# Performance work log

Measured on AMD Instinct MI355X. Metric: run time of the kernel, lower is better.

The kernel has to match this reference:

```python
import jax, jax.numpy as jnp
import numpy as np

N_NODES = 50000
N_EDGES = 800000
D_IN = 256
D_HID = 256
N_CLASSES = 10
N_GRAPHS = 512
LN_EPS = 1e-5


def gcn_conv(x, edge_index, W, b, num_nodes):
    # PyG GCNConv (default settings): h = x @ W; add self-loops; symmetric
    # deg^{-1/2} normalization; sum-aggregate messages; add bias.
    h = x @ W                                   # [N, H]
    loop = jnp.arange(num_nodes, dtype=edge_index.dtype)
    src = jnp.concatenate([edge_index[0], loop])  # [E+N]
    dst = jnp.concatenate([edge_index[1], loop])  # [E+N]
    deg = jax.ops.segment_sum(jnp.ones_like(dst, dtype=h.dtype), dst,
                              num_segments=num_nodes)
    dinv = jnp.where(deg > 0, jax.lax.rsqrt(deg), 0.0)
    norm = dinv[src] * dinv[dst]                # [E+N]
    msg = h[src] * norm[:, None]                # gather + scale
    out = jax.ops.segment_sum(msg, dst, num_segments=num_nodes)  # scatter-add
    return out + b


def layer_norm(x, w, b):
    mu = jnp.mean(x, axis=-1, keepdims=True)
    var = jnp.mean(jnp.square(x - mu), axis=-1, keepdims=True)
    return (x - mu) * jax.lax.rsqrt(var + LN_EPS) * w + b


def global_mean_pool(x, batch, num_graphs):
    s = jax.ops.segment_sum(x, batch, num_segments=num_graphs)
    cnt = jax.ops.segment_sum(jnp.ones_like(batch, dtype=x.dtype), batch,
                              num_segments=num_graphs)
    return s / jnp.maximum(cnt, 1.0)[:, None]


def setup_inputs() -> dict:
    key = jax.random.key(0)
    ks = jax.random.split(key, 12)
    x = jax.random.normal(ks[0], (N_NODES, D_IN), dtype=jnp.float32)
    edge_index = jax.random.randint(ks[1], (2, N_EDGES), 0, N_NODES, dtype=jnp.int32)
    batch = jnp.sort(jax.random.randint(ks[2], (N_NODES,), 0, N_GRAPHS, dtype=jnp.int32))
    s_in = 1.0 / np.sqrt(D_IN)
    s_hid = 1.0 / np.sqrt(D_HID)
    return {
        "x": x,
        "edge_index": edge_index,
        "batch": batch,
        "W1": jax.random.uniform(ks[3], (D_IN, D_HID), jnp.float32, -s_in, s_in),
        "b1": jnp.zeros((D_HID,), jnp.float32),
        "W2": jax.random.uniform(ks[4], (D_HID, D_HID), jnp.float32, -s_hid, s_hid),
        "b2": jnp.zeros((D_HID,), jnp.float32),
        "ln1_w": jnp.ones((D_HID,), jnp.float32),
        "ln1_b": jnp.zeros((D_HID,), jnp.float32),
        "ln2_w": jnp.ones((D_HID,), jnp.float32),
        "ln2_b": jnp.zeros((D_HID,), jnp.float32),
        "lin_W": jax.random.uniform(ks[5], (D_HID, N_CLASSES), jnp.float32, -s_hid, s_hid),
        "lin_b": jnp.zeros((N_CLASSES,), jnp.float32),
    }


def reference(x, edge_index, batch, W1, b1, W2, b2, ln1_w, ln1_b, ln2_w, ln2_b, lin_W, lin_b):
    # dropout is identity at inference (training=False)
    h = gcn_conv(x, edge_index, W1, b1, N_NODES)
    h = jax.nn.relu(layer_norm(h, ln1_w, ln1_b))
    h = gcn_conv(h, edge_index, W2, b2, N_NODES)
    h = jax.nn.relu(layer_norm(h, ln2_w, ln2_b))
    pooled = global_mean_pool(h, batch, N_GRAPHS)   # [G, H]
    return pooled @ lin_W + lin_b                   # [G, C]
```

## Files before the change

### kernel.cpp

```cpp
#include <hip/hip_runtime.h>
#include <hip/hip_fp8.h>
#include <stdint.h>

#define D 256
#define CAP 64

typedef __attribute__((ext_vector_type(8))) short short8;
typedef __attribute__((ext_vector_type(4))) float f32x4;

#define SW2(n, c) (((n) << 7) + ((((c) ^ ((n) & 7))) << 3))

__device__ inline unsigned short f2bf(float f) {
    uint32_t u = __builtin_bit_cast(uint32_t, f);
    uint32_t r = (u + 0x7FFFu + ((u >> 16) & 1u)) >> 16;
    return (unsigned short)r;
}

__device__ inline float bf2f(unsigned short b) {
    return __builtin_bit_cast(float, (uint32_t)b << 16);
}

__device__ inline f32x4 fp8x4_to_f32(uint32_t v) {
    __hip_fp8x4_e4m3 a;
    a.__x = v;
    float4 f = (float4)a;
    return (f32x4){f.x, f.y, f.z, f.w};
}

__device__ inline uint8_t f32_to_fp8(float f) {
    __hip_fp8_e4m3 q(f);
    return (uint8_t)q.__x;
}

__global__ __launch_bounds__(256) void k_prep(const float* __restrict__ x,
                                              unsigned short* __restrict__ xb, int n8,
                                              const float* __restrict__ W1,
                                              const float* __restrict__ W2,
                                              unsigned short* __restrict__ Wt1,
                                              unsigned short* __restrict__ Wt2,
                                              int* __restrict__ cur,
                                              int nNodes, int nf2b) {
    int b = blockIdx.x, t = threadIdx.x;
    if (b < nf2b) {
        int i = b * 256 + t;
        if (i < n8) {
            f32x4 v0 = ((const f32x4*)x)[i * 2];
            f32x4 v1 = ((const f32x4*)x)[i * 2 + 1];
            short8 o;
            o[0] = (short)f2bf(v0.x); o[1] = (short)f2bf(v0.y);
            o[2] = (short)f2bf(v0.z); o[3] = (short)f2bf(v0.w);
            o[4] = (short)f2bf(v1.x); o[5] = (short)f2bf(v1.y);
            o[6] = (short)f2bf(v1.z); o[7] = (short)f2bf(v1.w);
            ((short8*)xb)[i] = o;
        }
    } else if (b < nf2b + 512) {
        int idx = (b - nf2b) * 256 + t;
        int w = idx >> 16;
        int r = idx & 65535;
        int n = r >> 8, k = r & 255;
        const float* W = w ? W2 : W1;
        unsigned short* Wt = w ? Wt2 : Wt1;
        Wt[n * 256 + k] = f2bf(W[k * 256 + n]);
    } else {
        int i = (b - nf2b - 512) * 256 + t;
        if (i < nNodes) cur[i] = 0;
    }
}


__device__ __forceinline__ void gemm_body(unsigned short* sm, int gid,
                                          const unsigned short* __restrict__ A,
                                          const unsigned short* __restrict__ Bt,
                                          uint8_t* __restrict__ Cb, int M) {
    int t = threadIdx.x;
    int wave = t >> 6, lane = t & 63;
    int quad = lane >> 4, l16 = lane & 15;
    int mr = wave >> 1, nc = wave & 1;
    int bm = (gid >> 1) * 128;
    int bn = (gid & 1) * 128;

    uint4 af[4][8];
#pragma unroll
    for (int tm = 0; tm < 4; ++tm) {
        int row = bm + mr * 64 + tm * 16 + l16;
        if (row >= M) row = M - 1;
        const unsigned short* ap = A + (size_t)row * D + quad * 8;
#pragma unroll
        for (int ks = 0; ks < 8; ++ks)
            af[tm][ks] = *reinterpret_cast<const uint4*>(ap + ks * 32);
    }

    f32x4 acc[4][4];
#pragma unroll
    for (int tm = 0; tm < 4; ++tm)
#pragma unroll
        for (int tn = 0; tn < 4; ++tn) acc[tm][tn] = (f32x4){0.f, 0.f, 0.f, 0.f};

#pragma unroll
    for (int half = 0; half < 2; ++half) {
        {
            int c = t & 15;
            int r0 = t >> 4;
#pragma unroll
            for (int j = 0; j < 8; ++j) {
                int r = r0 + j * 16;
                uint4 v = *reinterpret_cast<const uint4*>(
                    Bt + (size_t)(bn + r) * D + half * 128 + c * 8);
                *reinterpret_cast<uint4*>(sm + SW2(r, c)) = v;
            }
        }
        __syncthreads();
#pragma unroll
        for (int ks = 0; ks < 4; ++ks) {
            int gks = half * 4 + ks;
            short8 b[4];
#pragma unroll
            for (int tn = 0; tn < 4; ++tn) {
                int n = nc * 64 + tn * 16 + l16;
                b[tn] = *reinterpret_cast<const short8*>(sm + SW2(n, ks * 4 + quad));
            }
#pragma unroll
            for (int tm = 0; tm < 4; ++tm) {
                short8 a = __builtin_bit_cast(short8, af[tm][gks]);
#pragma unroll
                for (int tn = 0; tn < 4; ++tn)
                    acc[tm][tn] = __builtin_amdgcn_mfma_f32_16x16x32_bf16(a, b[tn], acc[tm][tn], 0, 0, 0);
            }
        }
        __syncthreads();
    }

    uint8_t (*sC)[136] = reinterpret_cast<uint8_t (*)[136]>(sm);
#pragma unroll
    for (int tm = 0; tm < 4; ++tm) {
        int rb = mr * 64 + tm * 16 + quad * 4;
#pragma unroll
        for (int tn = 0; tn < 4; ++tn) {
            int cc = nc * 64 + tn * 16 + l16;
#pragma unroll
            for (int r = 0; r < 4; ++r)
                sC[rb + r][cc] = f32_to_fp8(acc[tm][tn][r]);
        }
    }
    __syncthreads();

#pragma unroll
    for (int it = 0; it < 4; ++it) {
        int idx = it * 256 + t;
        int r = idx >> 3, ch = idx & 7;
        int gr = bm + r;
        if (gr < M)
            *reinterpret_cast<uint4*>(Cb + (size_t)gr * D + bn + ch * 16) =
                *reinterpret_cast<const uint4*>(&sC[r][ch * 16]);
    }
}

__device__ __forceinline__ void fill_body(int fid,
                                          const int* __restrict__ src,
                                          const int* __restrict__ dst,
                                          int* __restrict__ cur,
                                          int* __restrict__ ewi, int ne) {
    int i = (fid * 256 + threadIdx.x) * 4;
    if (i + 4 <= ne) {
        int4 s4 = *reinterpret_cast<const int4*>(src + i);
        int4 d4 = *reinterpret_cast<const int4*>(dst + i);
        int p;
        p = atomicAdd(&cur[d4.x], 1);
        if (p < CAP) ewi[d4.x * CAP + p] = s4.x;
        p = atomicAdd(&cur[d4.y], 1);
        if (p < CAP) ewi[d4.y * CAP + p] = s4.y;
        p = atomicAdd(&cur[d4.z], 1);
        if (p < CAP) ewi[d4.z * CAP + p] = s4.z;
        p = atomicAdd(&cur[d4.w], 1);
        if (p < CAP) ewi[d4.w * CAP + p] = s4.w;
    } else {
        for (int j = i; j < ne; ++j) {
            int s = src[j], d = dst[j];
            int p = atomicAdd(&cur[d], 1);
            if (p < CAP) ewi[d * CAP + p] = s;
        }
    }
}

__global__ __launch_bounds__(256, 2) void k_gemmfill(const unsigned short* __restrict__ A,
                                                     const unsigned short* __restrict__ Bt,
                                                     uint8_t* __restrict__ Cb, int M,
                                                     const int* __restrict__ src,
                                                     const int* __restrict__ dst,
                                                     int* __restrict__ cur,
                                                     int* __restrict__ ewi, int ne,
                                                     int NI, int ngemm) {
    __shared__ unsigned short sm[16384];
    int b = blockIdx.x;
    if (b < 2 * NI) {
        if (b & 1) fill_body(b >> 1, src, dst, cur, ewi, ne);
        else       gemm_body(sm, b >> 1, A, Bt, Cb, M);
    } else {
        int r = b - 2 * NI;
        if (ngemm > NI) gemm_body(sm, NI + r, A, Bt, Cb, M);
        else            fill_body(NI + r, src, dst, cur, ewi, ne);
    }
}

__global__ __launch_bounds__(256, 2) void k_gemm(const unsigned short* __restrict__ A,
                                                 const unsigned short* __restrict__ Bt,
                                                 uint8_t* __restrict__ Cb, int M) {
    __shared__ unsigned short sm[16384];
    gemm_body(sm, blockIdx.x, A, Bt, Cb, M);
}

__global__ __launch_bounds__(256) void k_agg(const uint8_t* __restrict__ hb,
                                             const int* __restrict__ cur,
                                             const int* __restrict__ ewi,
                                             const float* __restrict__ bias,
                                             const float* __restrict__ lnw,
                                             const float* __restrict__ lnb,
                                             unsigned short* __restrict__ out, int n) {
    __shared__ int2 lew[4][CAP];
    int wave = threadIdx.x >> 6, lane = threadIdx.x & 63;
    int node = blockIdx.x * 4 + wave;
    if (node >= n) return;
    int cdeg = cur[node];
    int cnt = min(cdeg, CAP);
    if (lane < cnt) {
        int s = ewi[node * CAP + lane];
        int2 p;
        p.x = s * 64;
        p.y = __builtin_bit_cast(int, rsqrtf((float)(cur[s] + 1)));
        lew[wave][lane] = p;
    }
    __builtin_amdgcn_wave_barrier();

    float di = rsqrtf((float)(cdeg + 1));
    const uint32_t* hb32 = (const uint32_t*)hb;
    uint32_t rs = hb32[(uint32_t)node * 64 + lane];
    f32x4 acc = (f32x4){0.f, 0.f, 0.f, 0.f};
    const int2* lep = lew[wave];
    int nq = cnt >> 2;

    int2 p0, p1, p2, p3;
    if (nq > 0) { p0 = lep[0]; p1 = lep[1]; p2 = lep[2]; p3 = lep[3]; }
    int q = 0;
#pragma unroll 1
    for (; q + 1 < nq; ++q) {
        int b4 = (q + 1) * 4;
        uint32_t r0 = hb32[(uint32_t)(p0.x + lane)];
        uint32_t r1 = hb32[(uint32_t)(p1.x + lane)];
        uint32_t r2 = hb32[(uint32_t)(p2.x + lane)];
        uint32_t r3 = hb32[(uint32_t)(p3.x + lane)];
        int2 n0 = lep[b4], n1 = lep[b4 + 1], n2 = lep[b4 + 2], n3 = lep[b4 + 3];
        acc += fp8x4_to_f32(r0) * __builtin_bit_cast(float, p0.y);
        acc += fp8x4_to_f32(r1) * __builtin_bit_cast(float, p1.y);
        acc += fp8x4_to_f32(r2) * __builtin_bit_cast(float, p2.y);
        acc += fp8x4_to_f32(r3) * __builtin_bit_cast(float, p3.y);
        p0 = n0; p1 = n1; p2 = n2; p3 = n3;
    }
    if (nq > 0) {
        uint32_t r0 = hb32[(uint32_t)(p0.x + lane)];
        uint32_t r1 = hb32[(uint32_t)(p1.x + lane)];
        uint32_t r2 = hb32[(uint32_t)(p2.x + lane)];
        uint32_t r3 = hb32[(uint32_t)(p3.x + lane)];
        acc += fp8x4_to_f32(r0) * __builtin_bit_cast(float, p0.y);
        acc += fp8x4_to_f32(r1) * __builtin_bit_cast(float, p1.y);
        acc += fp8x4_to_f32(r2) * __builtin_bit_cast(float, p2.y);
        acc += fp8x4_to_f32(r3) * __builtin_bit_cast(float, p3.y);
    }
    for (int e = nq * 4; e < cnt; ++e) {
        int2 p = lep[e];
        uint32_t r = hb32[(uint32_t)(p.x + lane)];
        acc += fp8x4_to_f32(r) * __builtin_bit_cast(float, p.y);
    }

    f32x4 self = fp8x4_to_f32(rs);
    f32x4 b4v = ((const f32x4*)bias)[lane];
    f32x4 v = self * (di * di) + acc * di + b4v;

    float s1 = v.x + v.y + v.z + v.w;
    float s2 = v.x * v.x + v.y * v.y + v.z * v.z + v.w * v.w;
#pragma unroll
    for (int o = 32; o > 0; o >>= 1) {
        s1 += __shfl_xor(s1, o, 64);
        s2 += __shfl_xor(s2, o, 64);
    }
    float mean = s1 * (1.0f / 256.0f);
    float var = s2 * (1.0f / 256.0f) - mean * mean;
    float inv = rsqrtf(var + 1e-5f);
    f32x4 w4 = ((const f32x4*)lnw)[lane];
    f32x4 lb = ((const f32x4*)lnb)[lane];
    float y0 = fmaxf((v.x - mean) * inv * w4.x + lb.x, 0.f);
    float y1 = fmaxf((v.y - mean) * inv * w4.y + lb.y, 0.f);
    float y2 = fmaxf((v.z - mean) * inv * w4.z + lb.z, 0.f);
    float y3 = fmaxf((v.w - mean) * inv * w4.w + lb.w, 0.f);
    uint2 w;
    w.x = (uint32_t)f2bf(y0) | ((uint32_t)f2bf(y1) << 16);
    w.y = (uint32_t)f2bf(y2) | ((uint32_t)f2bf(y3) << 16);
    *reinterpret_cast<uint2*>(out + (size_t)node * D + lane * 4) = w;
}

__global__ __launch_bounds__(256) void k_pool(const unsigned short* __restrict__ h,
                                              const int* __restrict__ batch,
                                              const float* __restrict__ linW,
                                              const float* __restrict__ linb,
                                              float* __restrict__ out,
                                              int nNodes) {
    int g = blockIdx.x, t = threadIdx.x;
    int lo = 0, hi = nNodes;
    while (lo < hi) { int m = (lo + hi) >> 1; if (batch[m] < g) lo = m + 1; else hi = m; }
    int lo2 = lo, hi2 = nNodes;
    while (lo2 < hi2) { int m = (lo2 + hi2) >> 1; if (batch[m] < g + 1) lo2 = m + 1; else hi2 = m; }
    float s0 = 0.f, s1 = 0.f, s2 = 0.f, s3 = 0.f;
    int i = lo;
    for (; i + 4 <= lo2; i += 4) {
        s0 += bf2f(h[(size_t)(i + 0) * D + t]);
        s1 += bf2f(h[(size_t)(i + 1) * D + t]);
        s2 += bf2f(h[(size_t)(i + 2) * D + t]);
        s3 += bf2f(h[(size_t)(i + 3) * D + t]);
    }
    for (; i < lo2; ++i) s0 += bf2f(h[(size_t)i * D + t]);
    float s = (s0 + s1) + (s2 + s3);
    float cnt = (float)(lo2 - lo);
    float pooled = s / fmaxf(cnt, 1.f);
    __shared__ float sp[256];
    __shared__ float red[4];
    sp[t] = pooled;
    __syncthreads();
    for (int c = 0; c < 10; ++c) {
        float v = sp[t] * linW[t * 10 + c];
#pragma unroll
        for (int o = 32; o > 0; o >>= 1) v += __shfl_xor(v, o, 64);
        if ((t & 63) == 0) red[t >> 6] = v;
        __syncthreads();
        if (t == 0) out[g * 10 + c] = red[0] + red[1] + red[2] + red[3] + linb[c];
        __syncthreads();
    }
}

extern "C" void kernel_launch(void* const* d_in, const int* in_sizes, int n_in,
                              void* d_out, int out_size, void* d_ws, size_t ws_size,
                              hipStream_t stream) {
    const float* x    = (const float*)d_in[0];
    const int*   ei   = (const int*)d_in[1];
    const int*   batch= (const int*)d_in[2];
    const float* W1   = (const float*)d_in[3];
    const float* b1   = (const float*)d_in[4];
    const float* W2   = (const float*)d_in[5];
    const float* b2   = (const float*)d_in[6];
    const float* ln1w = (const float*)d_in[7];
    const float* ln1b = (const float*)d_in[8];
    const float* ln2w = (const float*)d_in[9];
    const float* ln2b = (const float*)d_in[10];
    const float* linW = (const float*)d_in[11];
    const float* linb = (const float*)d_in[12];
    float* out = (float*)d_out;

    int nNodes  = in_sizes[0] / D;
    int nEdges  = in_sizes[1] / 2;
    int nGraphs = out_size / 10;

    const int* src = ei;
    const int* dst = ei + nEdges;

    char* ws = (char*)d_ws;
    size_t o = 0;
    auto alloc = [&](size_t bytes) -> char* {
        char* p = ws + o;
        o += (bytes + 511) & ~(size_t)511;
        return p;
    };
    unsigned short* xb = (unsigned short*)alloc((size_t)nNodes * D * 2);
    uint8_t* hW = (uint8_t*)alloc((size_t)nNodes * D);
    unsigned short* h1 = (unsigned short*)alloc((size_t)nNodes * D * 2);
    int* cur   = (int*)alloc((size_t)nNodes * 4);
    int* ewi   = (int*)alloc((size_t)nNodes * CAP * 4);
    unsigned short* Wt1 = (unsigned short*)alloc((size_t)D * D * 2);
    unsigned short* Wt2 = (unsigned short*)alloc((size_t)D * D * 2);
    (void)ws_size;

    int gn = (nNodes + 255) / 256;
    int ge4 = (nEdges / 4 + 255) / 256;
    int n8 = nNodes * (D / 8);
    int nf2b = (n8 + 255) / 256;
    int ngemm = ((nNodes + 127) / 128) * 2;
    int NI = min(ngemm, ge4);

    k_prep<<<nf2b + 512 + gn, 256, 0, stream>>>(x, xb, n8, W1, W2, Wt1, Wt2,
                                                cur, nNodes, nf2b);
    k_gemmfill<<<ngemm + ge4, 256, 0, stream>>>(xb, Wt1, hW, nNodes,
                                                src, dst, cur, ewi, nEdges,
                                                NI, ngemm);
    k_agg<<<(nNodes + 3) / 4, 256, 0, stream>>>(hW, cur, ewi,
                                                b1, ln1w, ln1b, h1, nNodes);
    k_gemm<<<ngemm, 256, 0, stream>>>(h1, Wt2, hW, nNodes);
    k_agg<<<(nNodes + 3) / 4, 256, 0, stream>>>(hW, cur, ewi,
                                                b2, ln2w, ln2b, xb, nNodes);
    k_pool<<<nGraphs, 256, 0, stream>>>(xb, batch, linW, linb, out, nNodes);
}
```

Before: 269.6 us.

## Overlap edge fill with input conversion instead of with the first GEMM

Clearing the degree counters moves from the prep kernel to a hipMemsetAsync. The edge-bucketing fill now runs in one kernel alongside the x-to-bf16 conversion and weight transposes, instead of being interleaved with the first GEMM. The first GEMM becomes a plain k_gemm launch. The aim is to co-schedule the atomic-heavy fill with bandwidth-bound conversion work and let the GEMM run alone at its own occupancy, at the cost of one extra launch plus a memset.

```diff
diff --git a/kernel.cpp b/kernel.cpp
--- a/kernel.cpp
+++ b/kernel.cpp
@@ -30,129 +30,6 @@
 __device__ inline uint8_t f32_to_fp8(float f) {
     __hip_fp8_e4m3 q(f);
     return (uint8_t)q.__x;
-}
-
-__global__ __launch_bounds__(256) void k_prep(const float* __restrict__ x,
-                                              unsigned short* __restrict__ xb, int n8,
-                                              const float* __restrict__ W1,
-                                              const float* __restrict__ W2,
-                                              unsigned short* __restrict__ Wt1,
-                                              unsigned short* __restrict__ Wt2,
-                                              int* __restrict__ cur,
-                                              int nNodes, int nf2b) {
-    int b = blockIdx.x, t = threadIdx.x;
-    if (b < nf2b) {
-        int i = b * 256 + t;
-        if (i < n8) {
-            f32x4 v0 = ((const f32x4*)x)[i * 2];
-            f32x4 v1 = ((const f32x4*)x)[i * 2 + 1];
-            short8 o;
-            o[0] = (short)f2bf(v0.x); o[1] = (short)f2bf(v0.y);
-            o[2] = (short)f2bf(v0.z); o[3] = (short)f2bf(v0.w);
-            o[4] = (short)f2bf(v1.x); o[5] = (short)f2bf(v1.y);
-            o[6] = (short)f2bf(v1.z); o[7] = (short)f2bf(v1.w);
-            ((short8*)xb)[i] = o;
-        }
-    } else if (b < nf2b + 512) {
-        int idx = (b - nf2b) * 256 + t;
-        int w = idx >> 16;
-        int r = idx & 65535;
-        int n = r >> 8, k = r & 255;
-        const float* W = w ? W2 : W1;
-        unsigned short* Wt = w ? Wt2 : Wt1;
-        Wt[n * 256 + k] = f2bf(W[k * 256 + n]);
-    } else {
-        int i = (b - nf2b - 512) * 256 + t;
-        if (i < nNodes) cur[i] = 0;
-    }
-}
-
-
-__device__ __forceinline__ void gemm_body(unsigned short* sm, int gid,
-                                          const unsigned short* __restrict__ A,
-                                          const unsigned short* __restrict__ Bt,
-                                          uint8_t* __restrict__ Cb, int M) {
-    int t = threadIdx.x;
-    int wave = t >> 6, lane = t & 63;
-    int quad = lane >> 4, l16 = lane & 15;
-    int mr = wave >> 1, nc = wave & 1;
-    int bm = (gid >> 1) * 128;
-    int bn = (gid & 1) * 128;
-
-    uint4 af[4][8];
-#pragma unroll
-    for (int tm = 0; tm < 4; ++tm) {
-        int row = bm + mr * 64 + tm * 16 + l16;
-        if (row >= M) row = M - 1;
-        const unsigned short* ap = A + (size_t)row * D + quad * 8;
-#pragma unroll
-        for (int ks = 0; ks < 8; ++ks)
-            af[tm][ks] = *reinterpret_cast<const uint4*>(ap + ks * 32);
-    }
-
-    f32x4 acc[4][4];
-#pragma unroll
-    for (int tm = 0; tm < 4; ++tm)
-#pragma unroll
-        for (int tn = 0; tn < 4; ++tn) acc[tm][tn] = (f32x4){0.f, 0.f, 0.f, 0.f};
-
-#pragma unroll
-    for (int half = 0; half < 2; ++half) {
-        {
-            int c = t & 15;
-            int r0 = t >> 4;
-#pragma unroll
-            for (int j = 0; j < 8; ++j) {
-                int r = r0 + j * 16;
-                uint4 v = *reinterpret_cast<const uint4*>(
-                    Bt + (size_t)(bn + r) * D + half * 128 + c * 8);
-                *reinterpret_cast<uint4*>(sm + SW2(r, c)) = v;
-            }
-        }
-        __syncthreads();
-#pragma unroll
-        for (int ks = 0; ks < 4; ++ks) {
-            int gks = half * 4 + ks;
-            short8 b[4];
-#pragma unroll
-            for (int tn = 0; tn < 4; ++tn) {
-                int n = nc * 64 + tn * 16 + l16;
-                b[tn] = *reinterpret_cast<const short8*>(sm + SW2(n, ks * 4 + quad));
-            }
-#pragma unroll
-            for (int tm = 0; tm < 4; ++tm) {
-                short8 a = __builtin_bit_cast(short8, af[tm][gks]);
-#pragma unroll
-                for (int tn = 0; tn < 4; ++tn)
-                    acc[tm][tn] = __builtin_amdgcn_mfma_f32_16x16x32_bf16(a, b[tn], acc[tm][tn], 0, 0, 0);
-            }
-        }
-        __syncthreads();
-    }
-
-    uint8_t (*sC)[136] = reinterpret_cast<uint8_t (*)[136]>(sm);
-#pragma unroll
-    for (int tm = 0; tm < 4; ++tm) {
-        int rb = mr * 64 + tm * 16 + quad * 4;
-#pragma unroll
-        for (int tn = 0; tn < 4; ++tn) {
-            int cc = nc * 64 + tn * 16 + l16;
-#pragma unroll
-            for (int r = 0; r < 4; ++r)
-                sC[rb + r][cc] = f32_to_fp8(acc[tm][tn][r]);
-        }
-    }
-    __syncthreads();
-
-#pragma unroll
-    for (int it = 0; it < 4; ++it) {
-        int idx = it * 256 + t;
-        int r = idx >> 3, ch = idx & 7;
-        int gr = bm + r;
-        if (gr < M)
-            *reinterpret_cast<uint4*>(Cb + (size_t)gr * D + bn + ch * 16) =
-                *reinterpret_cast<const uint4*>(&sC[r][ch * 16]);
-    }
 }
 
 __device__ __forceinline__ void fill_body(int fid,
@@ -182,23 +59,40 @@
     }
 }
 
-__global__ __launch_bounds__(256, 2) void k_gemmfill(const unsigned short* __restrict__ A,
-                                                     const unsigned short* __restrict__ Bt,
-                                                     uint8_t* __restrict__ Cb, int M,
-                                                     const int* __restrict__ src,
-                                                     const int* __restrict__ dst,
-                                                     int* __restrict__ cur,
-                                                     int* __restrict__ ewi, int ne,
-                                                     int NI, int ngemm) {
-    __shared__ unsigned short sm[16384];
-    int b = blockIdx.x;
-    if (b < 2 * NI) {
-        if (b & 1) fill_body(b >> 1, src, dst, cur, ewi, ne);
-        else       gemm_body(sm, b >> 1, A, Bt, Cb, M);
+__global__ __launch_bounds__(256) void k_prepfill(const int* __restrict__ src,
+                                                  const int* __restrict__ dst,
+                                                  int* __restrict__ cur,
+                                                  int* __restrict__ ewi, int ne,
+                                                  const float* __restrict__ x,
+                                                  unsigned short* __restrict__ xb, int n8,
+                                                  const float* __restrict__ W1,
+                                                  const float* __restrict__ W2,
+                                                  unsigned short* __restrict__ Wt1,
+                                                  unsigned short* __restrict__ Wt2,
+                                                  int nfill, int nf2b) {
+    int b = blockIdx.x, t = threadIdx.x;
+    if (b < nfill) {
+        fill_body(b, src, dst, cur, ewi, ne);
+    } else if (b < nfill + nf2b) {
+        int i = (b - nfill) * 256 + t;
+        if (i < n8) {
+            f32x4 v0 = ((const f32x4*)x)[i * 2];
+            f32x4 v1 = ((const f32x4*)x)[i * 2 + 1];
+            short8 o;
+            o[0] = (short)f2bf(v0.x); o[1] = (short)f2bf(v0.y);
+            o[2] = (short)f2bf(v0.z); o[3] = (short)f2bf(v0.w);
+            o[4] = (short)f2bf(v1.x); o[5] = (short)f2bf(v1.y);
+            o[6] = (short)f2bf(v1.z); o[7] = (short)f2bf(v1.w);
+            ((short8*)xb)[i] = o;
+        }
     } else {
-        int r = b - 2 * NI;
-        if (ngemm > NI) gemm_body(sm, NI + r, A, Bt, Cb, M);
-        else            fill_body(NI + r, src, dst, cur, ewi, ne);
+        int idx = (b - nfill - nf2b) * 256 + t;
+        int w = idx >> 16;
+        int r = idx & 65535;
+        int n = r >> 8, k = r & 255;
+        const float* W = w ? W2 : W1;
+        unsigned short* Wt = w ? Wt2 : Wt1;
+        Wt[n * 256 + k] = f2bf(W[k * 256 + n]);
     }
 }
 
@@ -206,7 +100,88 @@
                                                  const unsigned short* __restrict__ Bt,
                                                  uint8_t* __restrict__ Cb, int M) {
     __shared__ unsigned short sm[16384];
-    gemm_body(sm, blockIdx.x, A, Bt, Cb, M);
+    int gid = blockIdx.x;
+    int t = threadIdx.x;
+    int wave = t >> 6, lane = t & 63;
+    int quad = lane >> 4, l16 = lane & 15;
+    int mr = wave >> 1, nc = wave & 1;
+    int bm = (gid >> 1) * 128;
+    int bn = (gid & 1) * 128;
+
+    uint4 af[4][8];
+#pragma unroll
+    for (int tm = 0; tm < 4; ++tm) {
+        int row = bm + mr * 64 + tm * 16 + l16;
+        if (row >= M) row = M - 1;
+        const unsigned short* ap = A + (size_t)row * D + quad * 8;
+#pragma unroll
+        for (int ks = 0; ks < 8; ++ks)
+            af[tm][ks] = *reinterpret_cast<const uint4*>(ap + ks * 32);
+    }
+
+    f32x4 acc[4][4];
+#pragma unroll
+    for (int tm = 0; tm < 4; ++tm)
+#pragma unroll
+        for (int tn = 0; tn < 4; ++tn) acc[tm][tn] = (f32x4){0.f, 0.f, 0.f, 0.f};
+
+#pragma unroll
+    for (int half = 0; half < 2; ++half) {
+        {
+            int c = t & 15;
+            int r0 = t >> 4;
+#pragma unroll
+            for (int j = 0; j < 8; ++j) {
+                int r = r0 + j * 16;
+                uint4 v = *reinterpret_cast<const uint4*>(
+                    Bt + (size_t)(bn + r) * D + half * 128 + c * 8);
+                *reinterpret_cast<uint4*>(sm + SW2(r, c)) = v;
+            }
+        }
+        __syncthreads();
+#pragma unroll
+        for (int ks = 0; ks < 4; ++ks) {
+            int gks = half * 4 + ks;
+            short8 b[4];
+#pragma unroll
+            for (int tn = 0; tn < 4; ++tn) {
+                int n = nc * 64 + tn * 16 + l16;
+                b[tn] = *reinterpret_cast<const short8*>(sm + SW2(n, ks * 4 + quad));
+            }
+#pragma unroll
+            for (int tm = 0; tm < 4; ++tm) {
+                short8 a = __builtin_bit_cast(short8, af[tm][gks]);
+#pragma unroll
+                for (int tn = 0; tn < 4; ++tn)
+                    acc[tm][tn] = __builtin_amdgcn_mfma_f32_16x16x32_bf16(a, b[tn], acc[tm][tn], 0, 0, 0);
+            }
+        }
+        __syncthreads();
+    }
+
+    uint8_t (*sC)[136] = reinterpret_cast<uint8_t (*)[136]>(sm);
+#pragma unroll
+    for (int tm = 0; tm < 4; ++tm) {
+        int rb = mr * 64 + tm * 16 + quad * 4;
+#pragma unroll
+        for (int tn = 0; tn < 4; ++tn) {
+            int cc = nc * 64 + tn * 16 + l16;
+#pragma unroll
+            for (int r = 0; r < 4; ++r)
+                sC[rb + r][cc] = f32_to_fp8(acc[tm][tn][r]);
+        }
+    }
+    __syncthreads();
+
+#pragma unroll
+    for (int it = 0; it < 4; ++it) {
+        int idx = it * 256 + t;
+        int r = idx >> 3, ch = idx & 7;
+        int gr = bm + r;
+        if (gr < M)
+            *reinterpret_cast<uint4*>(Cb + (size_t)gr * D + bn + ch * 16) =
+                *reinterpret_cast<const uint4*>(&sC[r][ch * 16]);
+    }
 }
 
 __global__ __launch_bounds__(256) void k_agg(const uint8_t* __restrict__ hb,
@@ -376,18 +351,16 @@
     unsigned short* Wt2 = (unsigned short*)alloc((size_t)D * D * 2);
     (void)ws_size;
 
-    int gn = (nNodes + 255) / 256;
     int ge4 = (nEdges / 4 + 255) / 256;
     int n8 = nNodes * (D / 8);
     int nf2b = (n8 + 255) / 256;
     int ngemm = ((nNodes + 127) / 128) * 2;
-    int NI = min(ngemm, ge4);
-
-    k_prep<<<nf2b + 512 + gn, 256, 0, stream>>>(x, xb, n8, W1, W2, Wt1, Wt2,
-                                                cur, nNodes, nf2b);
-    k_gemmfill<<<ngemm + ge4, 256, 0, stream>>>(xb, Wt1, hW, nNodes,
-                                                src, dst, cur, ewi, nEdges,
-                                                NI, ngemm);
+
+    hipMemsetAsync(cur, 0, (size_t)nNodes * 4, stream);
+    k_prepfill<<<ge4 + nf2b + 512, 256, 0, stream>>>(src, dst, cur, ewi, nEdges,
+                                                     x, xb, n8, W1, W2, Wt1, Wt2,
+                                                     ge4, nf2b);
+    k_gemm<<<ngemm, 256, 0, stream>>>(xb, Wt1, hW, nNodes);
     k_agg<<<(nNodes + 3) / 4, 256, 0, stream>>>(hW, cur, ewi,
                                                 b1, ln1w, ln1b, h1, nNodes);
     k_gemm<<<ngemm, 256, 0, stream>>>(h1, Wt2, hW, nNodes);
```

Result: slower. 321.3 us (+19.2%).
